# Kernel optimization log

Hardware: AMD Instinct MI355X
Metric: run time of the kernel (lower is better)

The kernel has to match this reference:

```python
import jax, jax.numpy as jnp
import numpy as np

N_NODES = 30000
N_REL = 8
N_EDGES = 131072
IN_FEAT = 512
OUT_FEAT = 512


def setup_inputs() -> dict:
    key = jax.random.key(0)
    k1, k2, k3, k4, k5 = jax.random.split(key, 5)
    x = jax.random.normal(k1, (N_NODES, IN_FEAT), dtype=jnp.float32)
    # per-relation weights [R, in, out] (xavier-ish scale)
    weight = jax.random.normal(k2, (N_REL, IN_FEAT, OUT_FEAT), dtype=jnp.float32) * (2.0 / (IN_FEAT + OUT_FEAT)) ** 0.5
    loop_weight = jax.random.normal(k3, (IN_FEAT, OUT_FEAT), dtype=jnp.float32) * (2.0 / (IN_FEAT + OUT_FEAT)) ** 0.5
    h_bias = jnp.zeros((OUT_FEAT,), dtype=jnp.float32)
    src = jax.random.randint(k4, (N_REL, N_EDGES), 0, N_NODES, dtype=jnp.int32)
    dst = jax.random.randint(k5, (N_REL, N_EDGES), 0, N_NODES, dtype=jnp.int32)
    return {"x": x, "weight": weight, "loop_weight": loop_weight,
            "h_bias": h_bias, "src": src, "dst": dst}


def reference(x, weight, loop_weight, h_bias, src, dst):
    # Per-relation GraphConv(norm='right', weight=W_r):
    #   transform all node feats, gather on src, scatter-sum on dst,
    #   normalize by in-degree (clamped to 1). Relations summed (HeteroGraphConv 'sum').
    xw = jnp.einsum('ni,rio->rno', x, weight)  # [R, N, out]

    def per_rel(xw_r, src_r, dst_r):
        msgs = xw_r[src_r]  # [E, out] gathered messages
        agg = jax.ops.segment_sum(msgs, dst_r, num_segments=N_NODES)
        deg = jax.ops.segment_sum(jnp.ones_like(dst_r, dtype=xw_r.dtype), dst_r,
                                  num_segments=N_NODES)
        return agg / jnp.clip(deg, 1.0)[:, None]

    h = jax.vmap(per_rel)(xw, src, dst).sum(axis=0)  # [N, out]
    h = h + x @ loop_weight + h_bias  # self-loop + bias
    return jax.nn.relu(h)  # activation; dropout=0.0 -> identity
```

## Files before the change

kernel.cpp:

```cpp
#include <hip/hip_runtime.h>
#include <hip/hip_bf16.h>

#define N_NODES 30000
#define N_REL   8
#define N_EDGES 131072
#define FEAT    512
#define KTOT    4608
#define CAP     32

typedef __attribute__((ext_vector_type(8))) __bf16 v8bf;
typedef __attribute__((ext_vector_type(4))) __bf16 v4bf;
typedef __attribute__((ext_vector_type(4))) float  v4f;
typedef __attribute__((ext_vector_type(8))) unsigned short u16x8;

static __device__ __forceinline__ void load_lds16(const void* g, void* l) {
  __builtin_amdgcn_global_load_lds(
      (const __attribute__((address_space(1))) void*)g,
      (__attribute__((address_space(3))) void*)l, 16, 0, 0);
}

#define CONV_BLOCKS 15000
#define TR_BLOCKS   2304
#define CNT_BLOCKS  512
__global__ __launch_bounds__(256)
void k_prep(const float* __restrict__ x, const float* __restrict__ w,
            const float* __restrict__ lw, const int* __restrict__ src,
            const int* __restrict__ dst, __bf16* __restrict__ xbf,
            __bf16* __restrict__ Wt, int* __restrict__ cnt,
            unsigned short* __restrict__ slots) {
  __shared__ float t[32][33];
  const int b = blockIdx.x, tid = threadIdx.x;
  if (b < CONV_BLOCKS) {
    int i = b * 256 + tid;
    float4 v = ((const float4*)x)[i];
    v4bf o;
    o[0] = (__bf16)v.x; o[1] = (__bf16)v.y; o[2] = (__bf16)v.z; o[3] = (__bf16)v.w;
    ((v4bf*)xbf)[i] = o;
  } else if (b < CONV_BLOCKS + TR_BLOCKS) {
    int tb = b - CONV_BLOCKS;
    int k0 = (tb % 144) * 32, n0 = (tb / 144) * 32;
    int tx = tid & 31, ty = tid >> 5;
    #pragma unroll
    for (int q = 0; q < 4; ++q) {
      int k = k0 + ty + q * 8, n = n0 + tx;
      float v = (k < 4096) ? w[(size_t)k * 512 + n] : lw[(size_t)(k - 4096) * 512 + n];
      t[ty + q * 8][tx] = v;
    }
    __syncthreads();
    #pragma unroll
    for (int q = 0; q < 4; ++q) {
      int n = n0 + ty + q * 8, k = k0 + tx;
      Wt[(size_t)n * KTOT + k] = (__bf16)t[tx][ty + q * 8];
    }
  } else {
    int cb  = b - CONV_BLOCKS - TR_BLOCKS;
    int rel = cb & 7;
    int q   = cb >> 3;
    int e0  = rel * N_EDGES + (q * 256 + tid) * 8;
    int4 sa = *(const int4*)(src + e0), sb = *(const int4*)(src + e0 + 4);
    int4 da = *(const int4*)(dst + e0), db = *(const int4*)(dst + e0 + 4);
    int ss[8] = {sa.x, sa.y, sa.z, sa.w, sb.x, sb.y, sb.z, sb.w};
    int dd[8] = {da.x, da.y, da.z, da.w, db.x, db.y, db.z, db.w};
    int bb[8], pp[8];
    #pragma unroll
    for (int j = 0; j < 8; ++j) {
      bb[j] = rel * N_NODES + dd[j];
      pp[j] = atomicAdd(&cnt[bb[j]], 1);
    }
    #pragma unroll
    for (int j = 0; j < 8; ++j)
      if (pp[j] < CAP) slots[(size_t)bb[j] * CAP + pp[j]] = (unsigned short)ss[j];
  }
}

__global__ __launch_bounds__(256)
void k_aggregate(const __bf16* __restrict__ xbf, const int* __restrict__ cnt,
                 const unsigned short* __restrict__ slots,
                 __bf16* __restrict__ out, int nBuckets) {
  int w = (blockIdx.x * blockDim.x + threadIdx.x) >> 6;
  int lane = threadIdx.x & 63;
  if (w >= nBuckets) return;
  const unsigned short* sl = slots + (size_t)w * CAP;
  u16x8 qs[4];
  qs[0] = *(const u16x8*)(sl);
  qs[1] = *(const u16x8*)(sl + 8);
  qs[2] = *(const u16x8*)(sl + 16);
  qs[3] = *(const u16x8*)(sl + 24);
  int c = cnt[w];
  int cc = c < CAP ? c : CAP;
  const __bf16* xb = xbf + (size_t)lane * 8;
  float acc[8] = {0.f,0.f,0.f,0.f,0.f,0.f,0.f,0.f};
  #pragma unroll
  for (int g = 0; g < 4; ++g) {
    if (cc > g * 8) {
      int m = cc - g * 8;
      v8bf r[8];
      #pragma unroll
      for (int j = 0; j < 8; ++j)
        if (m > j) r[j] = *(const v8bf*)(xb + (size_t)qs[g][j] * FEAT);
      #pragma unroll
      for (int j = 0; j < 8; ++j)
        if (m > j) {
          #pragma unroll
          for (int t = 0; t < 8; ++t) acc[t] += (float)r[j][t];
        }
    }
  }
  float scale = 1.0f / (float)(c > 1 ? c : 1);
  v8bf o;
  #pragma unroll
  for (int t = 0; t < 8; ++t) o[t] = (__bf16)(acc[t] * scale);
  *(v8bf*)(out + (size_t)w * FEAT + lane * 8) = o;
}

template <bool ACCUM, bool FINAL>
__global__ __launch_bounds__(256, 4)
void k_gemm(const __bf16* __restrict__ A, size_t slabStride,
            const __bf16* __restrict__ Wt, int wtStride, int kTiles,
            const float* __restrict__ bias, float* __restrict__ C,
            int mtBase, int mtEnd) {
  __shared__ __align__(16) char smem[33792];
  __bf16* As = (__bf16*)smem;
  __bf16* Bs = (__bf16*)(smem + 16384);

  const int tid  = threadIdx.x;
  const int wave = tid >> 6;
  const int lane = tid & 63;
  const int lr = lane >> 3, lc = lane & 7;
  const int gcs = (lc ^ lr) * 8;
  const int quad = lane >> 4, l15 = lane & 15;
  const int wRow = wave >> 1, wCol = wave & 1;

  const int panel = blockIdx.x >> 5;
  const int w32   = blockIdx.x & 31;
  const int mtile = mtBase + panel * 8 + (w32 & 7);
  const int ntile = w32 >> 3;
  if (mtile >= mtEnd) return;
  const int mBase = mtile * 128;
  const int nBase = ntile * 128;

  v4f acc[4][4];
  #pragma unroll
  for (int i = 0; i < 4; ++i)
    #pragma unroll
    for (int j = 0; j < 4; ++j) acc[i][j] = (v4f){0.f, 0.f, 0.f, 0.f};

  for (int kt = 0; kt < kTiles; ++kt) {
    const int kk = kt * 64;
    const __bf16* aT = A + (size_t)(kk >> 9) * slabStride + (kk & 511);
    #pragma unroll
    for (int t = 0; t < 4; ++t) {
      int chunk = wave * 4 + t;
      int row = mBase + chunk * 8 + lr;
      if (row > N_NODES - 1) row = N_NODES - 1;
      load_lds16(aT + (size_t)row * FEAT + gcs, As + chunk * 512);
      int n = nBase + chunk * 8 + lr;
      load_lds16(Wt + (size_t)n * wtStride + kk + gcs, Bs + chunk * 512);
    }
    __syncthreads();
    #pragma unroll
    for (int ks = 0; ks < 2; ++ks) {
      const int q = ks * 4 + quad;
      v8bf af[4], bfr[4];
      #pragma unroll
      for (int mi = 0; mi < 4; ++mi) {
        int m = wRow * 64 + mi * 16 + l15;
        af[mi] = *(const v8bf*)(As + m * 64 + ((q ^ (m & 7)) * 8));
      }
      #pragma unroll
      for (int ni = 0; ni < 4; ++ni) {
        int n = wCol * 64 + ni * 16 + l15;
        bfr[ni] = *(const v8bf*)(Bs + n * 64 + ((q ^ (n & 7)) * 8));
      }
      #pragma unroll
      for (int mi = 0; mi < 4; ++mi)
        #pragma unroll
        for (int ni = 0; ni < 4; ++ni)
          acc[mi][ni] = __builtin_amdgcn_mfma_f32_16x16x32_bf16(af[mi], bfr[ni], acc[mi][ni], 0, 0, 0);
    }
    __syncthreads();
  }

  float* cbuf = (float*)smem;
  const int f4c  = tid & 31;
  const int colg = nBase + f4c * 4;
  v4f bias4 = (v4f){0.f, 0.f, 0.f, 0.f};
  if (FINAL) bias4 = *(const v4f*)(bias + colg);
  #pragma unroll
  for (int h = 0; h < 2; ++h) {
    if (wRow == h) {
      #pragma unroll
      for (int mi = 0; mi < 4; ++mi) {
        int r0 = mi * 16 + quad * 4;
        #pragma unroll
        for (int ni = 0; ni < 4; ++ni) {
          int c = wCol * 64 + ni * 16 + l15;
          #pragma unroll
          for (int e = 0; e < 4; ++e)
            cbuf[(r0 + e) * 132 + c] = acc[mi][ni][e];
        }
      }
    }
    __syncthreads();
    #pragma unroll
    for (int i = 0; i < 8; ++i) {
      int rh  = (tid >> 5) + 8 * i;
      int row = mBase + h * 64 + rh;
      if (row < N_NODES) {
        v4f v = *(const v4f*)(cbuf + rh * 132 + f4c * 4);
        size_t idx = (size_t)row * FEAT + colg;
        if (ACCUM) {
          v4f c0 = *(const v4f*)(C + idx);
          v += c0;
        }
        if (FINAL) {
          #pragma unroll
          for (int e = 0; e < 4; ++e) v[e] = fmaxf(v[e] + bias4[e], 0.f);
        }
        *(v4f*)(C + idx) = v;
      }
    }
    __syncthreads();
  }
}

extern "C" void kernel_launch(void* const* d_in, const int* in_sizes, int n_in,
                              void* d_out, int out_size, void* d_ws, size_t ws_size,
                              hipStream_t stream) {
  const float* x    = (const float*)d_in[0];
  const float* w    = (const float*)d_in[1];
  const float* lw   = (const float*)d_in[2];
  const float* bias = (const float*)d_in[3];
  const int*   src  = (const int*)d_in[4];
  const int*   dst  = (const int*)d_in[5];
  float* out = (float*)d_out;

  char* ws = (char*)d_ws;
  const size_t SLAB  = (size_t)N_NODES * FEAT;
  const size_t slabB = SLAB * 2;
  const size_t wtB   = (size_t)FEAT * KTOT * 2;
  const size_t cntB  = (size_t)N_REL * N_NODES * 4;
  const size_t slotB = (size_t)N_REL * N_NODES * CAP * 2;
  const size_t fixedB = wtB + cntB + slotB;

  __bf16*         Wt     = (__bf16*)ws;
  int*            cnt    = (int*)(ws + wtB);
  unsigned short* slots  = (unsigned short*)(ws + wtB + cntB);
  __bf16*         slabs  = (__bf16*)(ws + fixedB);

  int nSlab = (int)((ws_size - fixedB) / slabB);
  if (nSlab > 9) nSlab = 9;
  int g = nSlab - 1;
  if (g > 8) g = 8;
  if (g < 1) g = 1;
  __bf16* xbf = slabs + (size_t)g * SLAB;

  hipMemsetAsync(cnt, 0, cntB, stream);
  k_prep<<<CONV_BLOCKS + TR_BLOCKS + CNT_BLOCKS, 256, 0, stream>>>(
      x, w, lw, src, dst, xbf, Wt, cnt, slots);

  const int nMtiles = (N_NODES + 127) / 128;

  if (g == 8) {
    const int hB = (N_REL * N_NODES) / 2;
    k_aggregate<<<hB / 4, 256, 0, stream>>>(xbf, cnt, slots, slabs, hB);
    k_aggregate<<<hB / 4, 256, 0, stream>>>(xbf, cnt + hB,
                                            slots + (size_t)hB * CAP,
                                            slabs + (size_t)hB * FEAT, hB);
    const int grid = ((nMtiles + 7) / 8) * 32;
    k_gemm<false, true><<<grid, 256, 0, stream>>>(slabs, SLAB, Wt, KTOT,
                                                  KTOT / 64, bias, out, 0, nMtiles);
  } else {
    const int gemmGrid = ((nMtiles + 7) / 8) * 32;
    for (int r0 = 0; r0 < N_REL; r0 += g) {
      int gc2 = (N_REL - r0) < g ? (N_REL - r0) : g;
      k_aggregate<<<(gc2 * N_NODES) / 4, 256, 0, stream>>>(
          xbf, cnt + r0 * N_NODES, slots + (size_t)r0 * N_NODES * CAP,
          slabs, gc2 * N_NODES);
      if (r0 == 0)
        k_gemm<false, false><<<gemmGrid, 256, 0, stream>>>(
            slabs, SLAB, Wt + r0 * 512, KTOT, gc2 * 8, bias, out, 0, nMtiles);
      else
        k_gemm<true, false><<<gemmGrid, 256, 0, stream>>>(
            slabs, SLAB, Wt + r0 * 512, KTOT, gc2 * 8, bias, out, 0, nMtiles);
    }
    k_gemm<true, true><<<gemmGrid, 256, 0, stream>>>(xbf, SLAB, Wt + 4096, KTOT,
                                                     8, bias, out, 0, nMtiles);
  }
}
```

Before: 546.1 us.

## Use nontemporal loads/stores in aggregate and split pipeline into 7+1 relation passes

Aggregation kernel now reads slot/count data and writes its output with nontemporal hints, so these streamed-once buffers pollute the cache less. The host schedule drops the single 8-relation aggregate plus one full-K GEMM. It now aggregates 7 relations, runs a GEMM over those, then aggregates the last relation into slab 6 and runs a final GEMM over it together with the self-loop slab. This uses one fewer workspace slab and shortens the large GEMM, but adds a read-modify-write of the fp32 output in the second GEMM.

New measurement: 542.9 us. No clear change (-0.6%).

```diff
diff --git a/kernel.cpp b/kernel.cpp
--- a/kernel.cpp
+++ b/kernel.cpp
@@ -82,11 +82,11 @@
   if (w >= nBuckets) return;
   const unsigned short* sl = slots + (size_t)w * CAP;
   u16x8 qs[4];
-  qs[0] = *(const u16x8*)(sl);
-  qs[1] = *(const u16x8*)(sl + 8);
-  qs[2] = *(const u16x8*)(sl + 16);
-  qs[3] = *(const u16x8*)(sl + 24);
-  int c = cnt[w];
+  qs[0] = __builtin_nontemporal_load((const u16x8*)(sl));
+  qs[1] = __builtin_nontemporal_load((const u16x8*)(sl + 8));
+  qs[2] = __builtin_nontemporal_load((const u16x8*)(sl + 16));
+  qs[3] = __builtin_nontemporal_load((const u16x8*)(sl + 24));
+  int c = __builtin_nontemporal_load(cnt + w);
   int cc = c < CAP ? c : CAP;
   const __bf16* xb = xbf + (size_t)lane * 8;
   float acc[8] = {0.f,0.f,0.f,0.f,0.f,0.f,0.f,0.f};
@@ -110,7 +110,7 @@
   v8bf o;
   #pragma unroll
   for (int t = 0; t < 8; ++t) o[t] = (__bf16)(acc[t] * scale);
-  *(v8bf*)(out + (size_t)w * FEAT + lane * 8) = o;
+  __builtin_nontemporal_store(o, (v8bf*)(out + (size_t)w * FEAT + lane * 8));
 }
 
 template <bool ACCUM, bool FINAL>
@@ -249,9 +249,8 @@
   __bf16*         slabs  = (__bf16*)(ws + fixedB);
 
   int nSlab = (int)((ws_size - fixedB) / slabB);
-  if (nSlab > 9) nSlab = 9;
   int g = nSlab - 1;
-  if (g > 8) g = 8;
+  if (g > 7) g = 7;
   if (g < 1) g = 1;
   __bf16* xbf = slabs + (size_t)g * SLAB;
 
@@ -260,18 +259,20 @@
       x, w, lw, src, dst, xbf, Wt, cnt, slots);
 
   const int nMtiles = (N_NODES + 127) / 128;
-
-  if (g == 8) {
-    const int hB = (N_REL * N_NODES) / 2;
-    k_aggregate<<<hB / 4, 256, 0, stream>>>(xbf, cnt, slots, slabs, hB);
-    k_aggregate<<<hB / 4, 256, 0, stream>>>(xbf, cnt + hB,
-                                            slots + (size_t)hB * CAP,
-                                            slabs + (size_t)hB * FEAT, hB);
-    const int grid = ((nMtiles + 7) / 8) * 32;
-    k_gemm<false, true><<<grid, 256, 0, stream>>>(slabs, SLAB, Wt, KTOT,
-                                                  KTOT / 64, bias, out, 0, nMtiles);
+  const int gemmGrid = ((nMtiles + 7) / 8) * 32;
+
+  if (g == 7) {
+    k_aggregate<<<(7 * N_NODES) / 4, 256, 0, stream>>>(xbf, cnt, slots,
+                                                       slabs, 7 * N_NODES);
+    k_gemm<false, false><<<gemmGrid, 256, 0, stream>>>(
+        slabs, SLAB, Wt, KTOT, 3584 / 64, bias, out, 0, nMtiles);
+    k_aggregate<<<N_NODES / 4, 256, 0, stream>>>(
+        xbf, cnt + 7 * N_NODES, slots + (size_t)7 * N_NODES * CAP,
+        slabs + (size_t)6 * SLAB, N_NODES);
+    k_gemm<true, true><<<gemmGrid, 256, 0, stream>>>(
+        slabs + (size_t)6 * SLAB, SLAB, Wt + 3584, KTOT, 1024 / 64,
+        bias, out, 0, nMtiles);
   } else {
-    const int gemmGrid = ((nMtiles + 7) / 8) * 32;
     for (int r0 = 0; r0 < N_REL; r0 += g) {
       int gc2 = (N_REL - r0) < g ? (N_REL - r0) : g;
       k_aggregate<<<(gc2 * N_NODES) / 4, 256, 0, stream>>>(
```
